# Kernel tuning notes

Measured on AMD Instinct MI355X. Metric: run time of the kernel, lower is better.

Reference implementation:

```python
import jax, jax.numpy as jnp
import numpy as np

N = 50000
E = 500000
IN_F = 128
HEADS = 4
NEG_SLOPE = 0.2


def _gatv2_conv(x, src, dst, Wl, Wr, att, bias, concat):
    # PyG GATv2Conv (share_weights=False): x_l = lin_l(x) for source, x_r = lin_r(x) for target
    n = x.shape[0]
    H, C = att.shape
    xl = (x @ Wl.T).reshape(n, H, C)
    xr = (x @ Wr.T).reshape(n, H, C)
    # per-edge: e_ij = att . leaky_relu(xl[j] + xr[i])
    e = jax.nn.leaky_relu(xl[src] + xr[dst], negative_slope=NEG_SLOPE)  # [E,H,C]
    logit = jnp.einsum('ehc,hc->eh', e, att)  # [E,H]
    # segment softmax over destination node
    lmax = jax.ops.segment_max(logit, dst, num_segments=n)
    lmax = jnp.where(jnp.isfinite(lmax), lmax, 0.0)
    w = jnp.exp(logit - lmax[dst])
    denom = jax.ops.segment_sum(w, dst, num_segments=n)
    alpha = w / (denom[dst] + 1e-16)
    # weighted scatter-aggregate of source messages
    out = jax.ops.segment_sum(xl[src] * alpha[:, :, None], dst, num_segments=n)  # [N,H,C]
    if concat:
        return out.reshape(n, H * C) + bias
    return out.mean(axis=1) + bias


def setup_inputs() -> dict:
    key = jax.random.key(0)
    ks = jax.random.split(key, 11)
    s = 0.1
    x = jax.random.normal(ks[0], (N, IN_F), jnp.float32)
    edge_index = jax.random.randint(ks[1], (2, E), 0, N, dtype=jnp.int32)
    # layer 1: in=128 -> heads=4, C=32, concat -> out 128
    Wl1 = jax.random.normal(ks[2], (128, IN_F), jnp.float32) * s
    Wr1 = jax.random.normal(ks[3], (128, IN_F), jnp.float32) * s
    att1 = jax.random.normal(ks[4], (HEADS, 32), jnp.float32) * s
    b1 = jnp.zeros((128,), jnp.float32)
    # layer 2: in=128 -> heads=4, C=64, mean (concat=False) -> out 64
    Wl2 = jax.random.normal(ks[5], (256, 128), jnp.float32) * s
    Wr2 = jax.random.normal(ks[6], (256, 128), jnp.float32) * s
    att2 = jax.random.normal(ks[7], (HEADS, 64), jnp.float32) * s
    b2 = jnp.zeros((64,), jnp.float32)
    return {"x": x, "edge_index": edge_index, "Wl1": Wl1, "Wr1": Wr1, "att1": att1,
            "b1": b1, "Wl2": Wl2, "Wr2": Wr2, "att2": att2, "b2": b2}


def reference(x, edge_index, Wl1, Wr1, att1, b1, Wl2, Wr2, att2, b2):
    n = x.shape[0]
    loops = jnp.arange(n, dtype=edge_index.dtype)
    src = jnp.concatenate([edge_index[0], loops])  # PyG add_self_loops=True
    dst = jnp.concatenate([edge_index[1], loops])
    # dropout inactive (inference); forward body: elu between layers
    h = jax.nn.elu(_gatv2_conv(x, src, dst, Wl1, Wr1, att1, b1, concat=True))
    logits = _gatv2_conv(h, src, dst, Wl2, Wr2, att2, b2, concat=False)
    return logits
```

## Files before the change

### kernel.cpp

```cpp
#include <hip/hip_runtime.h>
#include <hip/hip_bf16.h>
#include <math.h>


typedef _Float16 half2v __attribute__((ext_vector_type(2)));
typedef _Float16 half4v __attribute__((ext_vector_type(4)));
typedef _Float16 half8v __attribute__((ext_vector_type(8)));
typedef float float4v __attribute__((ext_vector_type(4)));

template <int CTRL>
static __device__ __forceinline__ float dppadd(float x) {
  int y = __builtin_amdgcn_update_dpp(0, __float_as_int(x), CTRL, 0xf, 0xf, true);
  return x + __int_as_float(y);
}

static __device__ __forceinline__ float red4dpp(float p) {
  p = dppadd<0xB1>(p);
  p = dppadd<0x4E>(p);
  return p;
}

static __device__ __forceinline__ float red8dpp(float p) {
  p = dppadd<0xB1>(p);
  p = dppadd<0x4E>(p);
  p = dppadd<0x141>(p);
  return p;
}


__global__ void cvt_w_count_kernel(
    const float* __restrict__ wl1, const float* __restrict__ wr1,
    const float* __restrict__ wl2, const float* __restrict__ wr2,
    _Float16* __restrict__ wb,
    const int* __restrict__ dst, int* __restrict__ deg, int E) {
  int i = blockIdx.x * blockDim.x + threadIdx.x;
  int stride = gridDim.x * blockDim.x;
  int total = 24576 + E;
  for (; i < total; i += stride) {
    if (i < 24576) {
      int fj = i * 4;
      const float* src;
      int so;
      if (fj < 16384) { src = wl1; so = fj; }
      else if (fj < 32768) { src = wr1; so = fj - 16384; }
      else if (fj < 65536) { src = wl2; so = fj - 32768; }
      else { src = wr2; so = fj - 65536; }
      float4 v = *(const float4*)(src + so);
      half4v o = {(_Float16)v.x, (_Float16)v.y, (_Float16)v.z, (_Float16)v.w};
      *(half4v*)(wb + fj) = o;
    } else {
      atomicAdd(&deg[dst[i - 24576]], 1);
    }
  }
}


__global__ void partial_kernel(const int* __restrict__ deg, int* __restrict__ partial, int N) {
  int t = threadIdx.x;
  int i = blockIdx.x * 256 + t;
  int v = (i < N) ? deg[i] : 0;
  v += __shfl_xor(v, 1); v += __shfl_xor(v, 2); v += __shfl_xor(v, 4);
  v += __shfl_xor(v, 8); v += __shfl_xor(v, 16); v += __shfl_xor(v, 32);
  __shared__ int ws[4];
  if ((t & 63) == 0) ws[t >> 6] = v;
  __syncthreads();
  if (t == 0) partial[blockIdx.x] = ws[0] + ws[1] + ws[2] + ws[3];
}

__global__ void scan_final_kernel(const int* __restrict__ deg, const int* __restrict__ partial,
                                  int* __restrict__ row_ptr, int* __restrict__ cursor,
                                  int N, int E, int nb) {
  __shared__ int sp[256];
  __shared__ int s[256];
  int t = threadIdx.x;
  int pv = (t < nb) ? partial[t] : 0;
  sp[t] = pv;
  __syncthreads();
  for (int off = 1; off < 256; off <<= 1) {
    int u = (t >= off) ? sp[t - off] : 0;
    __syncthreads();
    sp[t] += u;
    __syncthreads();
  }
  int blockpre = (blockIdx.x > 0) ? sp[blockIdx.x - 1] : 0;
  int i = blockIdx.x * 256 + t;
  int v = (i < N) ? deg[i] : 0;
  s[t] = v;
  __syncthreads();
  for (int off = 1; off < 256; off <<= 1) {
    int u = (t >= off) ? s[t - off] : 0;
    __syncthreads();
    s[t] += u;
    __syncthreads();
  }
  int excl = s[t] - v + blockpre;
  if (i < N) {
    row_ptr[i] = excl;
    cursor[i] = excl;
  }
  if (blockIdx.x == 0 && t == 0) row_ptr[N] = E;
}

__global__ void fill_kernel(const int* __restrict__ src, const int* __restrict__ dst,
                            int* __restrict__ cursor, int* __restrict__ col, int E) {
  int i = blockIdx.x * blockDim.x + threadIdx.x;
  if (i < E) {
    int d = dst[i];
    int pos = atomicAdd(&cursor[d], 1);
    col[pos] = src[i];
  }
}

template <bool AF32>
__global__ __launch_bounds__(256) void gemm_mfma2(
    const void* __restrict__ Av, const _Float16* __restrict__ Wa,
    const _Float16* __restrict__ Wb, _Float16* __restrict__ Ca,
    _Float16* __restrict__ Cb, int N, int Oa, int ldC) {
  __shared__ _Float16 lds[32768];
  int t = threadIdx.x;
  int gbase = blockIdx.y * 256;
#pragma unroll
  for (int i = 0; i < 16; ++i) {
    int c = t + i * 256;
    int row = c >> 4, kc = c & 15;
    int grow = gbase + row;
    const _Float16* srcW =
        (grow < Oa) ? (Wa + (size_t)grow * 128) : (Wb + (size_t)(grow - Oa) * 128);
    half8v v = *(const half8v*)(srcW + kc * 8);
    int off16 = (row << 4) | (kc ^ (row & 7));
    *(half8v*)((char*)lds + (off16 << 4)) = v;
  }
  __syncthreads();
  int wv = t >> 6, lane = t & 63;
  int l15 = lane & 15, l4 = lane >> 4;
  int row0 = blockIdx.x * 64 + (wv & 1) * 32;
  int colw = (wv >> 1) * 128;
  int gc = gbase + colw;
  half8v xf[2][4];
#pragma unroll
  for (int rg = 0; rg < 2; ++rg) {
    int r = row0 + rg * 16 + l15;
    bool valid = r < N;
    if constexpr (AF32) {
      const float* Ar = (const float*)Av + (size_t)r * 128 + l4 * 8;
#pragma unroll
      for (int kk = 0; kk < 4; ++kk) {
        half8v z = {};
        if (valid) {
          float4 q0 = *(const float4*)(Ar + kk * 32);
          float4 q1 = *(const float4*)(Ar + kk * 32 + 4);
          z = half8v{(_Float16)q0.x, (_Float16)q0.y, (_Float16)q0.z, (_Float16)q0.w,
                     (_Float16)q1.x, (_Float16)q1.y, (_Float16)q1.z, (_Float16)q1.w};
        }
        xf[rg][kk] = z;
      }
    } else {
      const half8v* Ar = (const half8v*)((const _Float16*)Av + (size_t)r * 128 + l4 * 8);
#pragma unroll
      for (int kk = 0; kk < 4; ++kk) {
        half8v z = {};
        xf[rg][kk] = valid ? Ar[kk * 4] : z;
      }
    }
  }
  int wrow = colw + l15;
  float4v acc[2][8] = {};
#pragma unroll
  for (int kk = 0; kk < 4; ++kk) {
    int xorterm = ((kk * 4 + l4) ^ (l15 & 7)) << 4;
    const char* base = (const char*)lds + wrow * 256 + xorterm;
    half8v wf[8];
#pragma unroll
    for (int ot = 0; ot < 8; ++ot) wf[ot] = *(const half8v*)(base + ot * 4096);
#pragma unroll
    for (int ot = 0; ot < 8; ++ot) {
      acc[0][ot] = __builtin_amdgcn_mfma_f32_16x16x32_f16(wf[ot], xf[0][kk], acc[0][ot], 0, 0, 0);
      acc[1][ot] = __builtin_amdgcn_mfma_f32_16x16x32_f16(wf[ot], xf[1][kk], acc[1][ot], 0, 0, 0);
    }
  }
  bool isA = gc < Oa;
  _Float16* C = isA ? Ca : Cb;
  int cb = isA ? gc : gc - Oa;
#pragma unroll
  for (int rg = 0; rg < 2; ++rg) {
    int r = row0 + rg * 16 + l15;
    if (r < N) {
#pragma unroll
      for (int ot = 0; ot < 8; ++ot) {
        half4v o = {(_Float16)acc[rg][ot][0], (_Float16)acc[rg][ot][1],
                    (_Float16)acc[rg][ot][2], (_Float16)acc[rg][ot][3]};
        *(half4v*)(C + (size_t)r * ldC + cb + ot * 16 + l4 * 4) = o;
      }
    }
  }
}


__global__ __launch_bounds__(128) void agg1_kernel(
    const _Float16* __restrict__ xl, const _Float16* __restrict__ xr,
    const float* __restrict__ att, const float* __restrict__ bias,
    const int* __restrict__ row_ptr, const int* __restrict__ col,
    _Float16* __restrict__ hout, int N) {
  int wid = (blockIdx.x * blockDim.x + threadIdx.x) >> 6;
  int lane = threadIdx.x & 63;
  if (wid >= N) return;
  int eslot = lane >> 4, sub = lane & 15;
  const uint d0 = (uint)sub * 8u;
  const float L2E = 1.44269504f;
  half8v xrv = *(const half8v*)(xr + (((uint)wid << 7) | d0));
  float4 af0 = *(const float4*)(att + d0);
  float4 af1 = *(const float4*)(att + d0 + 4);
  half2v at4[4] = {{(_Float16)(af0.x * L2E), (_Float16)(af0.y * L2E)},
                   {(_Float16)(af0.z * L2E), (_Float16)(af0.w * L2E)},
                   {(_Float16)(af1.x * L2E), (_Float16)(af1.y * L2E)},
                   {(_Float16)(af1.z * L2E), (_Float16)(af1.w * L2E)}};
  half8v k8 = {(_Float16)0.2f, (_Float16)0.2f, (_Float16)0.2f, (_Float16)0.2f,
               (_Float16)0.2f, (_Float16)0.2f, (_Float16)0.2f, (_Float16)0.2f};
  int e0 = row_ptr[wid];
  int deg = row_ptr[wid + 1] - e0;
  const int* ecol = col + e0;
  float s = 0.f, a[8] = {};
  auto edge = [&](half8v v, bool valid) {
    half8v u = v + xrv;
    half8v lr = __builtin_elementwise_max(u, u * k8);
    float pA = __builtin_amdgcn_fdot2((half2v){lr[0], lr[1]}, at4[0], 0.f, false);
    pA = __builtin_amdgcn_fdot2((half2v){lr[2], lr[3]}, at4[1], pA, false);
    float pB = __builtin_amdgcn_fdot2((half2v){lr[4], lr[5]}, at4[2], 0.f, false);
    pB = __builtin_amdgcn_fdot2((half2v){lr[6], lr[7]}, at4[3], pB, false);
    float p = red4dpp(pA + pB);
    float w = valid ? exp2f(p) : 0.f;
    s += w;
#pragma unroll
    for (int k = 0; k < 8; ++k) a[k] = fmaf(w, (float)v[k], a[k]);
  };
  auto ld = [&](uint node) { return *(const half8v*)(xl + ((node << 7) | d0)); };
  edge(ld((uint)wid), eslot == 0);
  if (deg > 0) {
    int dm1 = deg - 1;
    half8v vA = ld((uint)ecol[min(eslot, dm1)]);
    half8v vB = ld((uint)ecol[min(eslot + 4, dm1)]);
    half8v vC = ld((uint)ecol[min(eslot + 8, dm1)]);
    int M = deg >> 2, pf = eslot + 12;
#pragma unroll 2
    for (int j = 0; j < M; ++j) {
      half8v vD = ld((uint)ecol[min(pf, dm1)]);
      edge(vA, true);
      vA = vB; vB = vC; vC = vD; pf += 4;
    }
    int T = deg & 3;
    if (T) edge(vA, eslot < T);
  }
  s += __shfl_xor(s, 16); s += __shfl_xor(s, 32);
#pragma unroll
  for (int k = 0; k < 8; ++k) {
    a[k] += __shfl_xor(a[k], 16);
    a[k] += __shfl_xor(a[k], 32);
  }
  float inv = 1.f / (s + 1e-16f);
  if (eslot == 0) {
    float4 b0 = *(const float4*)(bias + d0);
    float4 b1 = *(const float4*)(bias + d0 + 4);
    float bb[8] = {b0.x, b0.y, b0.z, b0.w, b1.x, b1.y, b1.z, b1.w};
    half8v o;
#pragma unroll
    for (int k = 0; k < 8; ++k) {
      float tv = a[k] * inv + bb[k];
      tv = tv > 0.f ? tv : __expf(tv) - 1.f;
      o[k] = (_Float16)tv;
    }
    *(half8v*)(hout + (((uint)wid << 7) | d0)) = o;
  }
}

__global__ __launch_bounds__(128) void agg2_kernel(
    const _Float16* __restrict__ xl, const _Float16* __restrict__ xr,
    const float* __restrict__ att, const float* __restrict__ bias,
    const int* __restrict__ row_ptr, const int* __restrict__ col,
    float* __restrict__ out, int N) {
  int wid = (blockIdx.x * blockDim.x + threadIdx.x) >> 6;
  int lane = threadIdx.x & 63;
  if (wid >= N) return;
  int eslot = lane >> 5, sub = lane & 31;
  const uint d0 = (uint)sub * 8u;
  const float L2E = 1.44269504f;
  const float SH = 10.f;
  half8v xrv = *(const half8v*)(xr + (((uint)wid << 8) | d0));
  float4 af0 = *(const float4*)(att + d0);
  float4 af1 = *(const float4*)(att + d0 + 4);
  half2v at[4] = {{(_Float16)(af0.x * L2E), (_Float16)(af0.y * L2E)},
                  {(_Float16)(af0.z * L2E), (_Float16)(af0.w * L2E)},
                  {(_Float16)(af1.x * L2E), (_Float16)(af1.y * L2E)},
                  {(_Float16)(af1.z * L2E), (_Float16)(af1.w * L2E)}};
  half8v k8 = {(_Float16)0.2f, (_Float16)0.2f, (_Float16)0.2f, (_Float16)0.2f,
               (_Float16)0.2f, (_Float16)0.2f, (_Float16)0.2f, (_Float16)0.2f};
  int e0 = row_ptr[wid];
  int deg = row_ptr[wid + 1] - e0;
  const int* ecol = col + e0;
  float s;
  half8v ach;
  {
    half8v v = *(const half8v*)(xl + (((uint)wid << 8) | d0));
    half8v u = v + xrv;
    half8v lr = __builtin_elementwise_max(u, u * k8);
    float p = __builtin_amdgcn_fdot2((half2v){lr[0], lr[1]}, at[0], 0.f, false);
    p = __builtin_amdgcn_fdot2((half2v){lr[2], lr[3]}, at[1], p, false);
    p = __builtin_amdgcn_fdot2((half2v){lr[4], lr[5]}, at[2], p, false);
    p = __builtin_amdgcn_fdot2((half2v){lr[6], lr[7]}, at[3], p, false);
    p = red8dpp(p);
    float w = (eslot == 0) ? exp2f(p - SH) : 0.f;
    s = w;
    _Float16 wh = (_Float16)w;
    half8v w8 = {wh, wh, wh, wh, wh, wh, wh, wh};
    ach = v * w8;
  }
  if (deg > 0) {
    int dm1 = deg - 1;
    int cA = ecol[min(eslot, dm1)];
    int cB = ecol[min(eslot + 2, dm1)];
    int cC = ecol[min(eslot + 4, dm1)];
    half8v vA = *(const half8v*)(xl + (((uint)cA << 8) | d0));
    half8v vB = *(const half8v*)(xl + (((uint)cB << 8) | d0));
    half8v vC = *(const half8v*)(xl + (((uint)cC << 8) | d0));
    int M = deg >> 1;
    int pf = eslot + 6;
#pragma unroll 3
    for (int j = 0; j < M; ++j) {
      int cD = ecol[min(pf, dm1)];
      half8v vD = *(const half8v*)(xl + (((uint)cD << 8) | d0));
      half8v u = vA + xrv;
      half8v lr = __builtin_elementwise_max(u, u * k8);
      float p = __builtin_amdgcn_fdot2((half2v){lr[0], lr[1]}, at[0], 0.f, false);
      p = __builtin_amdgcn_fdot2((half2v){lr[2], lr[3]}, at[1], p, false);
      p = __builtin_amdgcn_fdot2((half2v){lr[4], lr[5]}, at[2], p, false);
      p = __builtin_amdgcn_fdot2((half2v){lr[6], lr[7]}, at[3], p, false);
      p = red8dpp(p);
      float w = exp2f(p - SH);
      s += w;
      _Float16 wh = (_Float16)w;
      half8v w8 = {wh, wh, wh, wh, wh, wh, wh, wh};
      ach += vA * w8;
      vA = vB; vB = vC; vC = vD; pf += 2;
    }
    if (deg & 1) {
      half8v u = vA + xrv;
      half8v lr = __builtin_elementwise_max(u, u * k8);
      float p = __builtin_amdgcn_fdot2((half2v){lr[0], lr[1]}, at[0], 0.f, false);
      p = __builtin_amdgcn_fdot2((half2v){lr[2], lr[3]}, at[1], p, false);
      p = __builtin_amdgcn_fdot2((half2v){lr[4], lr[5]}, at[2], p, false);
      p = __builtin_amdgcn_fdot2((half2v){lr[6], lr[7]}, at[3], p, false);
      p = red8dpp(p);
      float w = (eslot == 0) ? exp2f(p - SH) : 0.f;
      s += w;
      _Float16 wh = (_Float16)w;
      half8v w8 = {wh, wh, wh, wh, wh, wh, wh, wh};
      ach += vA * w8;
    }
  }
  s += __shfl_xor(s, 32);
  float ac[8];
#pragma unroll
  for (int k = 0; k < 8; ++k) {
    ac[k] = (float)ach[k];
    ac[k] += __shfl_xor(ac[k], 32);
  }
  float inv = 1.f / (s + 1e-16f);
#pragma unroll
  for (int k = 0; k < 8; ++k) ac[k] *= inv;
#pragma unroll
  for (int k = 0; k < 8; ++k) {
    ac[k] += __shfl_xor(ac[k], 8);
    ac[k] += __shfl_xor(ac[k], 16);
  }
  if (lane < 8) {
    float4 b0 = *(const float4*)(bias + lane * 8);
    float4 b1v = *(const float4*)(bias + lane * 8 + 4);
    float4 o0 = make_float4(ac[0] * 0.25f + b0.x, ac[1] * 0.25f + b0.y,
                            ac[2] * 0.25f + b0.z, ac[3] * 0.25f + b0.w);
    float4 o1 = make_float4(ac[4] * 0.25f + b1v.x, ac[5] * 0.25f + b1v.y,
                            ac[6] * 0.25f + b1v.z, ac[7] * 0.25f + b1v.w);
    float* op = out + (size_t)wid * 64 + lane * 8;
    *(float4*)op = o0;
    *(float4*)(op + 4) = o1;
  }
}

extern "C" void kernel_launch(void* const* d_in, const int* in_sizes, int n_in,
                              void* d_out, int out_size, void* d_ws, size_t ws_size,
                              hipStream_t stream) {
  const float* x = (const float*)d_in[0];
  const int* ei = (const int*)d_in[1];
  const float* Wl1 = (const float*)d_in[2];
  const float* Wr1 = (const float*)d_in[3];
  const float* att1 = (const float*)d_in[4];
  const float* b1 = (const float*)d_in[5];
  const float* Wl2 = (const float*)d_in[6];
  const float* Wr2 = (const float*)d_in[7];
  const float* att2 = (const float*)d_in[8];
  const float* b2 = (const float*)d_in[9];
  float* out = (float*)d_out;

  int N = in_sizes[0] / 128;
  int E = in_sizes[1] / 2;
  const int* srcArr = ei;
  const int* dstArr = ei + E;

  char* w = (char*)d_ws;
  auto alloc = [&](size_t bytes) {
    char* p = w;
    w += (bytes + 255) & ~(size_t)255;
    return p;
  };
  int* row_ptr = (int*)alloc((size_t)(N + 1) * sizeof(int));
  int* cursor = (int*)alloc((size_t)N * sizeof(int));
  int* partial = (int*)alloc(256 * sizeof(int));
  int* col = (int*)alloc((size_t)E * sizeof(int));
  _Float16* wb = (_Float16*)alloc(98304 * 2);
  _Float16* hb = (_Float16*)alloc((size_t)N * 128 * 2);
  _Float16* xl1 = (_Float16*)alloc((size_t)N * 128 * 2);
  _Float16* xr1 = (_Float16*)alloc((size_t)N * 128 * 2);
  _Float16* xl2 = (_Float16*)alloc((size_t)N * 256 * 2);
  _Float16* xr2 = (_Float16*)alloc((size_t)N * 256 * 2);

  const _Float16* wl1b = wb;
  const _Float16* wr1b = wb + 16384;
  const _Float16* wl2b = wb + 32768;
  const _Float16* wr2b = wb + 65536;

  hipMemsetAsync(cursor, 0, (size_t)N * sizeof(int), stream);
  cvt_w_count_kernel<<<1024, 256, 0, stream>>>(Wl1, Wr1, Wl2, Wr2, wb, dstArr, cursor, E);

  int nb = (N + 255) / 256;
  partial_kernel<<<nb, 256, 0, stream>>>(cursor, partial, N);
  scan_final_kernel<<<nb, 256, 0, stream>>>(cursor, partial, row_ptr, cursor, N, E, nb);
  fill_kernel<<<(E + 255) / 256, 256, 0, stream>>>(srcArr, dstArr, cursor, col, E);

  int gx = (N + 63) / 64;
  int aggBlocks = (N * 64 + 127) / 128;
  gemm_mfma2<true><<<dim3(gx, 1), 256, 0, stream>>>(x, wl1b, wr1b, xl1, xr1, N, 128, 128);
  agg1_kernel<<<aggBlocks, 128, 0, stream>>>(xl1, xr1, att1, b1, row_ptr, col, hb, N);

  gemm_mfma2<false><<<dim3(gx, 2), 256, 0, stream>>>(hb, wl2b, wr2b, xl2, xr2, N, 256, 256);
  agg2_kernel<<<aggBlocks, 128, 0, stream>>>(xl2, xr2, att2, b2, row_ptr, col, out, N);
}
```

Measured before the change: 186.6 us.

## Keep GEMM weights in registers and loop persistently over row tiles

The GEMM kernel stops staging the full 256x128 weight slice in LDS for every 64-row block. Each wave now holds its own 64 output columns of weights in registers and the grid becomes persistent (512 blocks striding over row tiles), so weights are loaded once per wave instead of once per tile. This removes the LDS fill, the barrier and the LDS reads. In exchange it uses more registers (wfr 4x4 plus xf 4x4 plus acc) and the same A rows are now read by all four waves from global or cache.

```diff
diff --git a/kernel.cpp b/kernel.cpp
--- a/kernel.cpp
+++ b/kernel.cpp
@@ -112,84 +112,75 @@
 }
 
 template <bool AF32>
-__global__ __launch_bounds__(256) void gemm_mfma2(
+__global__ __launch_bounds__(256, 2) void gemm_reg(
     const void* __restrict__ Av, const _Float16* __restrict__ Wa,
     const _Float16* __restrict__ Wb, _Float16* __restrict__ Ca,
-    _Float16* __restrict__ Cb, int N, int Oa, int ldC) {
-  __shared__ _Float16 lds[32768];
-  int t = threadIdx.x;
-  int gbase = blockIdx.y * 256;
-#pragma unroll
-  for (int i = 0; i < 16; ++i) {
-    int c = t + i * 256;
-    int row = c >> 4, kc = c & 15;
-    int grow = gbase + row;
-    const _Float16* srcW =
-        (grow < Oa) ? (Wa + (size_t)grow * 128) : (Wb + (size_t)(grow - Oa) * 128);
-    half8v v = *(const half8v*)(srcW + kc * 8);
-    int off16 = (row << 4) | (kc ^ (row & 7));
-    *(half8v*)((char*)lds + (off16 << 4)) = v;
-  }
-  __syncthreads();
-  int wv = t >> 6, lane = t & 63;
+    _Float16* __restrict__ Cb, int N, int Oa, int ldC, int ntiles) {
+  int wv = threadIdx.x >> 6, lane = threadIdx.x & 63;
   int l15 = lane & 15, l4 = lane >> 4;
-  int row0 = blockIdx.x * 64 + (wv & 1) * 32;
-  int colw = (wv >> 1) * 128;
-  int gc = gbase + colw;
-  half8v xf[2][4];
-#pragma unroll
-  for (int rg = 0; rg < 2; ++rg) {
-    int r = row0 + rg * 16 + l15;
-    bool valid = r < N;
-    if constexpr (AF32) {
-      const float* Ar = (const float*)Av + (size_t)r * 128 + l4 * 8;
-#pragma unroll
-      for (int kk = 0; kk < 4; ++kk) {
-        half8v z = {};
-        if (valid) {
-          float4 q0 = *(const float4*)(Ar + kk * 32);
-          float4 q1 = *(const float4*)(Ar + kk * 32 + 4);
-          z = half8v{(_Float16)q0.x, (_Float16)q0.y, (_Float16)q0.z, (_Float16)q0.w,
-                     (_Float16)q1.x, (_Float16)q1.y, (_Float16)q1.z, (_Float16)q1.w};
+  int o0 = blockIdx.y * 256 + wv * 64;
+  bool isA = o0 < Oa;
+  const _Float16* W = isA ? Wa : Wb;
+  _Float16* C = isA ? Ca : Cb;
+  int wcb = isA ? o0 : o0 - Oa;
+  half8v wfr[4][4];
+#pragma unroll
+  for (int ot = 0; ot < 4; ++ot) {
+    const _Float16* Wr = W + (size_t)(wcb + ot * 16 + l15) * 128 + l4 * 8;
+#pragma unroll
+    for (int kk = 0; kk < 4; ++kk) wfr[ot][kk] = *(const half8v*)(Wr + kk * 32);
+  }
+  for (int rt = blockIdx.x; rt < ntiles; rt += gridDim.x) {
+    int row0 = rt * 64;
+    half8v xf[4][4];
+#pragma unroll
+    for (int rg = 0; rg < 4; ++rg) {
+      int r = row0 + rg * 16 + l15;
+      bool valid = r < N;
+      if constexpr (AF32) {
+        const float* Ar = (const float*)Av + (size_t)r * 128 + l4 * 8;
+#pragma unroll
+        for (int kk = 0; kk < 4; ++kk) {
+          half8v z = {};
+          if (valid) {
+            float4 q0 = *(const float4*)(Ar + kk * 32);
+            float4 q1 = *(const float4*)(Ar + kk * 32 + 4);
+            z = half8v{(_Float16)q0.x, (_Float16)q0.y, (_Float16)q0.z, (_Float16)q0.w,
+                       (_Float16)q1.x, (_Float16)q1.y, (_Float16)q1.z, (_Float16)q1.w};
+          }
+          xf[rg][kk] = z;
         }
-        xf[rg][kk] = z;
+      } else {
+        const _Float16* Ar = (const _Float16*)Av + (size_t)r * 128 + l4 * 8;
+#pragma unroll
+        for (int kk = 0; kk < 4; ++kk) {
+          half8v z = {};
+          xf[rg][kk] = valid ? *(const half8v*)(Ar + kk * 32) : z;
+        }
       }
-    } else {
-      const half8v* Ar = (const half8v*)((const _Float16*)Av + (size_t)r * 128 + l4 * 8);
-#pragma unroll
-      for (int kk = 0; kk < 4; ++kk) {
-        half8v z = {};
-        xf[rg][kk] = valid ? Ar[kk * 4] : z;
+    }
+    float4v acc[4][4] = {};
+#pragma unroll
+    for (int kk = 0; kk < 4; ++kk) {
+#pragma unroll
+      for (int ot = 0; ot < 4; ++ot) {
+#pragma unroll
+        for (int rg = 0; rg < 4; ++rg) {
+          acc[rg][ot] =
+              __builtin_amdgcn_mfma_f32_16x16x32_f16(wfr[ot][kk], xf[rg][kk], acc[rg][ot], 0, 0, 0);
+        }
       }
     }
-  }
-  int wrow = colw + l15;
-  float4v acc[2][8] = {};
-#pragma unroll
-  for (int kk = 0; kk < 4; ++kk) {
-    int xorterm = ((kk * 4 + l4) ^ (l15 & 7)) << 4;
-    const char* base = (const char*)lds + wrow * 256 + xorterm;
-    half8v wf[8];
-#pragma unroll
-    for (int ot = 0; ot < 8; ++ot) wf[ot] = *(const half8v*)(base + ot * 4096);
-#pragma unroll
-    for (int ot = 0; ot < 8; ++ot) {
-      acc[0][ot] = __builtin_amdgcn_mfma_f32_16x16x32_f16(wf[ot], xf[0][kk], acc[0][ot], 0, 0, 0);
-      acc[1][ot] = __builtin_amdgcn_mfma_f32_16x16x32_f16(wf[ot], xf[1][kk], acc[1][ot], 0, 0, 0);
-    }
-  }
-  bool isA = gc < Oa;
-  _Float16* C = isA ? Ca : Cb;
-  int cb = isA ? gc : gc - Oa;
-#pragma unroll
-  for (int rg = 0; rg < 2; ++rg) {
-    int r = row0 + rg * 16 + l15;
-    if (r < N) {
-#pragma unroll
-      for (int ot = 0; ot < 8; ++ot) {
-        half4v o = {(_Float16)acc[rg][ot][0], (_Float16)acc[rg][ot][1],
-                    (_Float16)acc[rg][ot][2], (_Float16)acc[rg][ot][3]};
-        *(half4v*)(C + (size_t)r * ldC + cb + ot * 16 + l4 * 4) = o;
+#pragma unroll
+    for (int rg = 0; rg < 4; ++rg) {
+      int r = row0 + rg * 16 + l15;
+      if (r < N) {
+#pragma unroll
+        for (int ot = 0; ot < 4; ++ot) {
+          half4v o = {(_Float16)acc[rg][ot][0], (_Float16)acc[rg][ot][1],
+                      (_Float16)acc[rg][ot][2], (_Float16)acc[rg][ot][3]};
+          *(half4v*)(C + (size_t)r * ldC + wcb + ot * 16 + l4 * 4) = o;
+        }
       }
     }
   }
@@ -434,11 +425,11 @@
   scan_final_kernel<<<nb, 256, 0, stream>>>(cursor, partial, row_ptr, cursor, N, E, nb);
   fill_kernel<<<(E + 255) / 256, 256, 0, stream>>>(srcArr, dstArr, cursor, col, E);
 
-  int gx = (N + 63) / 64;
+  int ntiles = (N + 63) / 64;
   int aggBlocks = (N * 64 + 127) / 128;
-  gemm_mfma2<true><<<dim3(gx, 1), 256, 0, stream>>>(x, wl1b, wr1b, xl1, xr1, N, 128, 128);
+  gemm_reg<true><<<dim3(512, 1), 256, 0, stream>>>(x, wl1b, wr1b, xl1, xr1, N, 128, 128, ntiles);
   agg1_kernel<<<aggBlocks, 128, 0, stream>>>(xl1, xr1, att1, b1, row_ptr, col, hb, N);
 
-  gemm_mfma2<false><<<dim3(gx, 2), 256, 0, stream>>>(hb, wl2b, wr2b, xl2, xr2, N, 256, 256);
+  gemm_reg<false><<<dim3(512, 2), 256, 0, stream>>>(hb, wl2b, wr2b, xl2, xr2, N, 256, 256, ntiles);
   agg2_kernel<<<aggBlocks, 128, 0, stream>>>(xl2, xr2, att2, b2, row_ptr, col, out, N);
 }
```

Result: slower. 200.2 us (+7.3%).

## Fuse CSR construction into one cooperative kernel and convert weights inside GEMM

Applied to the files above, without the earlier changes.

The memset, degree count, two scan kernels and fill kernel are merged into a single cooperative kernel of 512 blocks, with grid.sync between phases. The separate weight fp32-to-fp16 conversion pass is dropped, and the GEMM now loads fp32 weights and converts them while staging into LDS. The aim is to cut launch overhead and the gaps between kernels. In exchange it adds grid-wide barriers and repeats the weight conversion in every GEMM block. The scan phase also assumes nchunks (196) fits within both the 512 blocks and the 256-entry partial scan.

```diff
diff --git a/kernel.cpp b/kernel.cpp
--- a/kernel.cpp
+++ b/kernel.cpp
@@ -1,6 +1,9 @@
 #include <hip/hip_runtime.h>
 #include <hip/hip_bf16.h>
+#include <hip/hip_cooperative_groups.h>
 #include <math.h>
+
+namespace cg = cooperative_groups;
 
 
 typedef _Float16 half2v __attribute__((ext_vector_type(2)));
@@ -28,93 +31,71 @@
 }
 
 
-__global__ void cvt_w_count_kernel(
-    const float* __restrict__ wl1, const float* __restrict__ wr1,
-    const float* __restrict__ wl2, const float* __restrict__ wr2,
-    _Float16* __restrict__ wb,
-    const int* __restrict__ dst, int* __restrict__ deg, int E) {
-  int i = blockIdx.x * blockDim.x + threadIdx.x;
-  int stride = gridDim.x * blockDim.x;
-  int total = 24576 + E;
-  for (; i < total; i += stride) {
-    if (i < 24576) {
-      int fj = i * 4;
-      const float* src;
-      int so;
-      if (fj < 16384) { src = wl1; so = fj; }
-      else if (fj < 32768) { src = wr1; so = fj - 16384; }
-      else if (fj < 65536) { src = wl2; so = fj - 32768; }
-      else { src = wr2; so = fj - 65536; }
-      float4 v = *(const float4*)(src + so);
-      half4v o = {(_Float16)v.x, (_Float16)v.y, (_Float16)v.z, (_Float16)v.w};
-      *(half4v*)(wb + fj) = o;
-    } else {
-      atomicAdd(&deg[dst[i - 24576]], 1);
-    }
-  }
-}
-
-
-__global__ void partial_kernel(const int* __restrict__ deg, int* __restrict__ partial, int N) {
+__global__ void csr_coop(const int* __restrict__ src, const int* __restrict__ dst,
+                         int* __restrict__ degc, int* __restrict__ partial,
+                         int* __restrict__ row_ptr, int* __restrict__ col,
+                         int N, int E, int nchunks) {
+  cg::grid_group grid = cg::this_grid();
+  int tid = blockIdx.x * blockDim.x + threadIdx.x;
+  int gs = gridDim.x * blockDim.x;
   int t = threadIdx.x;
-  int i = blockIdx.x * 256 + t;
-  int v = (i < N) ? deg[i] : 0;
-  v += __shfl_xor(v, 1); v += __shfl_xor(v, 2); v += __shfl_xor(v, 4);
-  v += __shfl_xor(v, 8); v += __shfl_xor(v, 16); v += __shfl_xor(v, 32);
-  __shared__ int ws[4];
-  if ((t & 63) == 0) ws[t >> 6] = v;
-  __syncthreads();
-  if (t == 0) partial[blockIdx.x] = ws[0] + ws[1] + ws[2] + ws[3];
-}
-
-__global__ void scan_final_kernel(const int* __restrict__ deg, const int* __restrict__ partial,
-                                  int* __restrict__ row_ptr, int* __restrict__ cursor,
-                                  int N, int E, int nb) {
-  __shared__ int sp[256];
-  __shared__ int s[256];
-  int t = threadIdx.x;
-  int pv = (t < nb) ? partial[t] : 0;
-  sp[t] = pv;
-  __syncthreads();
-  for (int off = 1; off < 256; off <<= 1) {
-    int u = (t >= off) ? sp[t - off] : 0;
+  for (int i = tid; i < N; i += gs) degc[i] = 0;
+  grid.sync();
+  for (int i = tid; i < E; i += gs) atomicAdd(&degc[dst[i]], 1);
+  grid.sync();
+  if (blockIdx.x < nchunks) {
+    int i = blockIdx.x * 256 + t;
+    int v = (i < N) ? degc[i] : 0;
+    v += __shfl_xor(v, 1); v += __shfl_xor(v, 2); v += __shfl_xor(v, 4);
+    v += __shfl_xor(v, 8); v += __shfl_xor(v, 16); v += __shfl_xor(v, 32);
+    __shared__ int ws[4];
+    if ((t & 63) == 0) ws[t >> 6] = v;
     __syncthreads();
-    sp[t] += u;
+    if (t == 0) partial[blockIdx.x] = ws[0] + ws[1] + ws[2] + ws[3];
+  }
+  grid.sync();
+  if (blockIdx.x < nchunks) {
+    __shared__ int sp[256];
+    __shared__ int s[256];
+    int pv = (t < nchunks) ? partial[t] : 0;
+    sp[t] = pv;
     __syncthreads();
-  }
-  int blockpre = (blockIdx.x > 0) ? sp[blockIdx.x - 1] : 0;
-  int i = blockIdx.x * 256 + t;
-  int v = (i < N) ? deg[i] : 0;
-  s[t] = v;
-  __syncthreads();
-  for (int off = 1; off < 256; off <<= 1) {
-    int u = (t >= off) ? s[t - off] : 0;
+    for (int off = 1; off < 256; off <<= 1) {
+      int u = (t >= off) ? sp[t - off] : 0;
+      __syncthreads();
+      sp[t] += u;
+      __syncthreads();
+    }
+    int blockpre = (blockIdx.x > 0) ? sp[blockIdx.x - 1] : 0;
+    int i = blockIdx.x * 256 + t;
+    int v = (i < N) ? degc[i] : 0;
+    s[t] = v;
     __syncthreads();
-    s[t] += u;
-    __syncthreads();
-  }
-  int excl = s[t] - v + blockpre;
-  if (i < N) {
-    row_ptr[i] = excl;
-    cursor[i] = excl;
-  }
-  if (blockIdx.x == 0 && t == 0) row_ptr[N] = E;
-}
-
-__global__ void fill_kernel(const int* __restrict__ src, const int* __restrict__ dst,
-                            int* __restrict__ cursor, int* __restrict__ col, int E) {
-  int i = blockIdx.x * blockDim.x + threadIdx.x;
-  if (i < E) {
+    for (int off = 1; off < 256; off <<= 1) {
+      int u = (t >= off) ? s[t - off] : 0;
+      __syncthreads();
+      s[t] += u;
+      __syncthreads();
+    }
+    int excl = s[t] - v + blockpre;
+    if (i < N) {
+      row_ptr[i] = excl;
+      degc[i] = excl;
+    }
+    if (blockIdx.x == 0 && t == 0) row_ptr[N] = E;
+  }
+  grid.sync();
+  for (int i = tid; i < E; i += gs) {
     int d = dst[i];
-    int pos = atomicAdd(&cursor[d], 1);
+    int pos = atomicAdd(&degc[d], 1);
     col[pos] = src[i];
   }
 }
 
 template <bool AF32>
 __global__ __launch_bounds__(256) void gemm_mfma2(
-    const void* __restrict__ Av, const _Float16* __restrict__ Wa,
-    const _Float16* __restrict__ Wb, _Float16* __restrict__ Ca,
+    const void* __restrict__ Av, const float* __restrict__ Wa,
+    const float* __restrict__ Wb, _Float16* __restrict__ Ca,
     _Float16* __restrict__ Cb, int N, int Oa, int ldC) {
   __shared__ _Float16 lds[32768];
   int t = threadIdx.x;
@@ -124,9 +105,12 @@
     int c = t + i * 256;
     int row = c >> 4, kc = c & 15;
     int grow = gbase + row;
-    const _Float16* srcW =
+    const float* srcW =
         (grow < Oa) ? (Wa + (size_t)grow * 128) : (Wb + (size_t)(grow - Oa) * 128);
-    half8v v = *(const half8v*)(srcW + kc * 8);
+    float4 q0 = *(const float4*)(srcW + kc * 8);
+    float4 q1 = *(const float4*)(srcW + kc * 8 + 4);
+    half8v v = {(_Float16)q0.x, (_Float16)q0.y, (_Float16)q0.z, (_Float16)q0.w,
+                (_Float16)q1.x, (_Float16)q1.y, (_Float16)q1.z, (_Float16)q1.w};
     int off16 = (row << 4) | (kc ^ (row & 7));
     *(half8v*)((char*)lds + (off16 << 4)) = v;
   }
@@ -155,11 +139,11 @@
         xf[rg][kk] = z;
       }
     } else {
-      const half8v* Ar = (const half8v*)((const _Float16*)Av + (size_t)r * 128 + l4 * 8);
+      const _Float16* Ar = (const _Float16*)Av + (size_t)r * 128 + l4 * 8;
 #pragma unroll
       for (int kk = 0; kk < 4; ++kk) {
         half8v z = {};
-        xf[rg][kk] = valid ? Ar[kk * 4] : z;
+        xf[rg][kk] = valid ? *(const half8v*)(Ar + kk * 32) : z;
       }
     }
   }
@@ -414,31 +398,24 @@
   int* cursor = (int*)alloc((size_t)N * sizeof(int));
   int* partial = (int*)alloc(256 * sizeof(int));
   int* col = (int*)alloc((size_t)E * sizeof(int));
-  _Float16* wb = (_Float16*)alloc(98304 * 2);
   _Float16* hb = (_Float16*)alloc((size_t)N * 128 * 2);
   _Float16* xl1 = (_Float16*)alloc((size_t)N * 128 * 2);
   _Float16* xr1 = (_Float16*)alloc((size_t)N * 128 * 2);
   _Float16* xl2 = (_Float16*)alloc((size_t)N * 256 * 2);
   _Float16* xr2 = (_Float16*)alloc((size_t)N * 256 * 2);
 
-  const _Float16* wl1b = wb;
-  const _Float16* wr1b = wb + 16384;
-  const _Float16* wl2b = wb + 32768;
-  const _Float16* wr2b = wb + 65536;
-
-  hipMemsetAsync(cursor, 0, (size_t)N * sizeof(int), stream);
-  cvt_w_count_kernel<<<1024, 256, 0, stream>>>(Wl1, Wr1, Wl2, Wr2, wb, dstArr, cursor, E);
-
-  int nb = (N + 255) / 256;
-  partial_kernel<<<nb, 256, 0, stream>>>(cursor, partial, N);
-  scan_final_kernel<<<nb, 256, 0, stream>>>(cursor, partial, row_ptr, cursor, N, E, nb);
-  fill_kernel<<<(E + 255) / 256, 256, 0, stream>>>(srcArr, dstArr, cursor, col, E);
+  int nchunks = (N + 255) / 256;
+  {
+    void* args[] = {(void*)&srcArr, (void*)&dstArr, (void*)&cursor, (void*)&partial,
+                    (void*)&row_ptr, (void*)&col, (void*)&N, (void*)&E, (void*)&nchunks};
+    hipLaunchCooperativeKernel((void*)csr_coop, dim3(512), dim3(256), args, 0, stream);
+  }
 
   int gx = (N + 63) / 64;
   int aggBlocks = (N * 64 + 127) / 128;
-  gemm_mfma2<true><<<dim3(gx, 1), 256, 0, stream>>>(x, wl1b, wr1b, xl1, xr1, N, 128, 128);
+  gemm_mfma2<true><<<dim3(gx, 1), 256, 0, stream>>>(x, Wl1, Wr1, xl1, xr1, N, 128, 128);
   agg1_kernel<<<aggBlocks, 128, 0, stream>>>(xl1, xr1, att1, b1, row_ptr, col, hb, N);
 
-  gemm_mfma2<false><<<dim3(gx, 2), 256, 0, stream>>>(hb, wl2b, wr2b, xl2, xr2, N, 256, 256);
+  gemm_mfma2<false><<<dim3(gx, 2), 256, 0, stream>>>(hb, Wl2, Wr2, xl2, xr2, N, 256, 256);
   agg2_kernel<<<aggBlocks, 128, 0, stream>>>(xl2, xr2, att2, b2, row_ptr, col, out, N);
 }
```

New measurement: 394.5 us. +111.5%, slower.
